# Kernel tuning notes

Measured on AMD Instinct MI355X. Metric: run time of the kernel, lower is better.

## Reference

```python
import jax, jax.numpy as jnp
import numpy as np

K = 8
NEG = -1e16


def setup_inputs() -> dict:
    key = jax.random.key(0)
    inputs = jax.random.normal(key, (1048576, 64), dtype=jnp.float32)
    return {"inputs": inputs}


def reference(inputs) -> jnp.ndarray:
    depth = inputs.shape[1]
    # top-k along last axis (values unused; only indices form the mask)
    _, top_k_indices = jax.lax.top_k(inputs, K)            # [N, K]
    # sum of one-hots -> membership mask [N, depth]
    one_hot = jax.nn.one_hot(top_k_indices, depth, dtype=inputs.dtype)  # [N, K, depth]
    mask = jnp.sum(one_hot, axis=1)                        # [N, depth]
    sparse_inputs = jnp.where(mask > 0.0, inputs, jnp.full_like(inputs, NEG))
    return jax.nn.softmax(sparse_inputs, axis=1)
```

## Files before the change

kernel.cpp:

```cpp
#include <hip/hip_runtime.h>
#include <math.h>


#define D4 16
#define ROWS 32
#define TILE_F4 (ROWS * D4)
#define WAVES 2
#define THREADS (WAVES * 64)

#define LVL(ti) { const float _hi = fmaxf(ti, _a); _a = fminf(ti, _a); ti = _hi; }
#define INSERT(x) { float _a = (x); \
    LVL(t0) LVL(t1) LVL(t2) LVL(t3) LVL(t4) LVL(t5) LVL(t6) \
    t7 = fmaxf(t7, _a); }

#define PROC(x, o) { \
    const int _kgt = ((x) > thr); \
    const int _keq = ((x) == thr) & (quota > 0); \
    quota -= _keq; \
    (o) = (_kgt | _keq) ? __expf((x) - m) * inv : 0.0f; }

__device__ __forceinline__ void gload_lds16(const void* g, void* l) {
    __builtin_amdgcn_global_load_lds(
        (__attribute__((address_space(1))) void*)(g),
        (__attribute__((address_space(3))) void*)(l),
        16, 0, 0);
}

__global__ __launch_bounds__(THREADS)
void topk_softmax_kernel(const float* __restrict__ in,
                         float* __restrict__ out,
                         int ntiles)
{
    __shared__ float4 tile_[WAVES][TILE_F4];

    const int lane = threadIdx.x & 63;
    const int wid  = threadIdx.x >> 6;
    const int w = blockIdx.x * WAVES + wid;
    if (w >= ntiles) return;
    float4* tile = tile_[wid];

    const float4* __restrict__ p = reinterpret_cast<const float4*>(in) + (long long)w * TILE_F4;
    float4* __restrict__ q       = reinterpret_cast<float4*>(out)      + (long long)w * TILE_F4;

    const int g = lane >> 4;
    const int s = lane & 15;

    #pragma unroll
    for (int c = 0; c < 8; ++c) {
        const int r = c * 4 + g;
        const int k = s ^ (r & 15);
        gload_lds16(p + r * 16 + k, tile + c * 64);
    }
    asm volatile("s_waitcnt vmcnt(0)" ::: "memory");

    const int half = lane >> 5;
    const int r    = lane & 31;
    const int kbase = half << 3;
    const int rk = r & 15;
    float4 v[8];
    #pragma unroll
    for (int c = 0; c < 8; ++c) v[c] = tile[r * 16 + ((kbase + c) ^ rk)];

    float t0 = -INFINITY, t1 = -INFINITY, t2 = -INFINITY, t3 = -INFINITY,
          t4 = -INFINITY, t5 = -INFINITY, t6 = -INFINITY, t7 = -INFINITY;
    #pragma unroll
    for (int c = 0; c < 8; ++c) {
        INSERT(v[c].x) INSERT(v[c].y) INSERT(v[c].z) INSERT(v[c].w)
    }

    const float p0 = __shfl_xor(t0, 32), p1 = __shfl_xor(t1, 32),
                p2 = __shfl_xor(t2, 32), p3 = __shfl_xor(t3, 32),
                p4 = __shfl_xor(t4, 32), p5 = __shfl_xor(t5, 32),
                p6 = __shfl_xor(t6, 32), p7 = __shfl_xor(t7, 32);
    const float c0 = fmaxf(t0, p7), c1 = fmaxf(t1, p6), c2 = fmaxf(t2, p5),
                c3 = fmaxf(t3, p4), c4 = fmaxf(t4, p3), c5 = fmaxf(t5, p2),
                c6 = fmaxf(t6, p1), c7 = fmaxf(t7, p0);
    const float m   = fmaxf(t0, p0);
    const float thr = fminf(fminf(fminf(c0, c1), fminf(c2, c3)),
                            fminf(fminf(c4, c5), fminf(c6, c7)));
    const int cnt_gt = (c0 > thr) + (c1 > thr) + (c2 > thr) + (c3 > thr) +
                       (c4 > thr) + (c5 > thr) + (c6 > thr) + (c7 > thr);
    const float sum = __expf(c0 - m) + __expf(c1 - m) + __expf(c2 - m) + __expf(c3 - m) +
                      __expf(c4 - m) + __expf(c5 - m) + __expf(c6 - m) + __expf(c7 - m);
    const float inv = 1.0f / sum;
    const int quota0 = 8 - cnt_gt;

    int ce = 0;
    #pragma unroll
    for (int c = 0; c < 8; ++c)
        ce += (v[c].x == thr) + (v[c].y == thr) + (v[c].z == thr) + (v[c].w == thr);
    const int ce_partner = __shfl_xor(ce, 32);
    int quota = half ? (quota0 - ce_partner) : quota0;

    #pragma unroll
    for (int c = 0; c < 8; ++c) {
        float4 o;
        PROC(v[c].x, o.x) PROC(v[c].y, o.y) PROC(v[c].z, o.z) PROC(v[c].w, o.w)
        tile[r * 16 + ((kbase + c) ^ rk)] = o;
    }
    asm volatile("s_waitcnt lgkmcnt(0)" ::: "memory");

    #pragma unroll
    for (int c = 0; c < 8; ++c) {
        const int rr = c * 4 + g;
        q[c * 64 + lane] = tile[rr * 16 + (s ^ (rr & 15))];
    }
}

__global__ __launch_bounds__(64)
void topk_softmax_tail(const float* __restrict__ in, float* __restrict__ out,
                       long long row0, long long nrows)
{
    const long long row = row0 + threadIdx.x;
    if (row >= nrows) return;
    const float4* __restrict__ p = reinterpret_cast<const float4*>(in) + row * D4;
    float4* __restrict__ q       = reinterpret_cast<float4*>(out)      + row * D4;
    float4 v[D4];
    #pragma unroll
    for (int c = 0; c < D4; ++c) v[c] = p[c];
    float t0 = -INFINITY, t1 = -INFINITY, t2 = -INFINITY, t3 = -INFINITY,
          t4 = -INFINITY, t5 = -INFINITY, t6 = -INFINITY, t7 = -INFINITY;
    #pragma unroll
    for (int c = 0; c < D4; ++c) {
        INSERT(v[c].x) INSERT(v[c].y) INSERT(v[c].z) INSERT(v[c].w)
    }
    const float thr = t7;
    const float m   = t0;
    int quota = 8 - ((t0 > thr) + (t1 > thr) + (t2 > thr) + (t3 > thr) +
                     (t4 > thr) + (t5 > thr) + (t6 > thr));
    const float sum = __expf(t0 - m) + __expf(t1 - m) + __expf(t2 - m) + __expf(t3 - m) +
                      __expf(t4 - m) + __expf(t5 - m) + __expf(t6 - m) + __expf(t7 - m);
    const float inv = 1.0f / sum;
    #pragma unroll
    for (int c = 0; c < D4; ++c) {
        float4 o;
        PROC(v[c].x, o.x) PROC(v[c].y, o.y) PROC(v[c].z, o.z) PROC(v[c].w, o.w)
        q[c] = o;
    }
}

extern "C" void kernel_launch(void* const* d_in, const int* in_sizes, int n_in,
                              void* d_out, int out_size, void* d_ws, size_t ws_size,
                              hipStream_t stream) {
    const float* in = (const float*)d_in[0];
    float* out = (float*)d_out;
    const long long nrows = in_sizes[0] / 64;
    const int ntiles = (int)(nrows / ROWS);
    const long long rem = nrows - (long long)ntiles * ROWS;

    if (ntiles > 0) {
        const int nblocks = (ntiles + WAVES - 1) / WAVES;
        topk_softmax_kernel<<<nblocks, THREADS, 0, stream>>>(in, out, ntiles);
    }
    if (rem > 0) {
        topk_softmax_tail<<<1, 64, 0, stream>>>(in, out, (long long)ntiles * ROWS, nrows);
    }
}
```

Before: 100.6 us.

## Use med3 top-k insertion, log-sum-exp scaling, tie fast path, nontemporal stores

Replaces the min/max insertion network with an fmed3-based sorted insertion, which needs fewer instructions per element. The reciprocal multiply becomes a single subtraction of m+log(sum) inside the exponent. Tie handling now uses a branch-free fast path and runs a slow quota path only when ties straddle the threshold. It also adds occupancy launch bounds and nontemporal output stores. The cost is extra code and small rounding differences from the log-based normalisation.

New measurement: 98.71 us. No clear change (-1.9%).

```diff
diff --git a/kernel.cpp b/kernel.cpp
--- a/kernel.cpp
+++ b/kernel.cpp
@@ -8,11 +8,30 @@
 #define WAVES 2
 #define THREADS (WAVES * 64)
 
+typedef float nfloat4 __attribute__((ext_vector_type(4)));
+
+#define INS(xx) { \
+    const float _x = (xx); \
+    const float n0 = fmaxf(t0, _x); \
+    const float n1 = __builtin_amdgcn_fmed3f(t0, t1, _x); \
+    const float n2 = __builtin_amdgcn_fmed3f(t1, t2, _x); \
+    const float n3 = __builtin_amdgcn_fmed3f(t2, t3, _x); \
+    const float n4 = __builtin_amdgcn_fmed3f(t3, t4, _x); \
+    const float n5 = __builtin_amdgcn_fmed3f(t4, t5, _x); \
+    const float n6 = __builtin_amdgcn_fmed3f(t5, t6, _x); \
+    const float n7 = __builtin_amdgcn_fmed3f(t6, t7, _x); \
+    t0 = n0; t1 = n1; t2 = n2; t3 = n3; t4 = n4; t5 = n5; t6 = n6; t7 = n7; }
+
+#define PROCF(x, o) { (o) = ((x) >= thr) ? __expf((x) - B) : 0.0f; }
+#define PROCS(x, o) { \
+    const int _k = ((x) == thr) & (quota > 0); \
+    quota -= _k; \
+    (o) = (((x) > thr) | _k) ? __expf((x) - B) : 0.0f; }
+
 #define LVL(ti) { const float _hi = fmaxf(ti, _a); _a = fminf(ti, _a); ti = _hi; }
 #define INSERT(x) { float _a = (x); \
     LVL(t0) LVL(t1) LVL(t2) LVL(t3) LVL(t4) LVL(t5) LVL(t6) \
     t7 = fmaxf(t7, _a); }
-
 #define PROC(x, o) { \
     const int _kgt = ((x) > thr); \
     const int _keq = ((x) == thr) & (quota > 0); \
@@ -26,7 +45,7 @@
         16, 0, 0);
 }
 
-__global__ __launch_bounds__(THREADS)
+__global__ __launch_bounds__(THREADS, 5)
 void topk_softmax_kernel(const float* __restrict__ in,
                          float* __restrict__ out,
                          int ntiles)
@@ -48,24 +67,26 @@
     #pragma unroll
     for (int c = 0; c < 8; ++c) {
         const int r = c * 4 + g;
-        const int k = s ^ (r & 15);
-        gload_lds16(p + r * 16 + k, tile + c * 64);
+        gload_lds16(p + r * 16 + (s ^ (r & 15)), tile + c * 64);
     }
     asm volatile("s_waitcnt vmcnt(0)" ::: "memory");
 
-    const int half = lane >> 5;
-    const int r    = lane & 31;
-    const int kbase = half << 3;
+    const int r  = lane & 31;
+    const int h  = lane >> 5;
     const int rk = r & 15;
+    int slot[8];
     float4 v[8];
     #pragma unroll
-    for (int c = 0; c < 8; ++c) v[c] = tile[r * 16 + ((kbase + c) ^ rk)];
+    for (int j = 0; j < 8; ++j) {
+        slot[j] = r * 16 + ((8 * h + j) ^ rk);
+        v[j] = tile[slot[j]];
+    }
 
     float t0 = -INFINITY, t1 = -INFINITY, t2 = -INFINITY, t3 = -INFINITY,
           t4 = -INFINITY, t5 = -INFINITY, t6 = -INFINITY, t7 = -INFINITY;
     #pragma unroll
-    for (int c = 0; c < 8; ++c) {
-        INSERT(v[c].x) INSERT(v[c].y) INSERT(v[c].z) INSERT(v[c].w)
+    for (int j = 0; j < 8; ++j) {
+        INS(v[j].x) INS(v[j].y) INS(v[j].z) INS(v[j].w)
     }
 
     const float p0 = __shfl_xor(t0, 32), p1 = __shfl_xor(t1, 32),
@@ -82,28 +103,51 @@
                        (c4 > thr) + (c5 > thr) + (c6 > thr) + (c7 > thr);
     const float sum = __expf(c0 - m) + __expf(c1 - m) + __expf(c2 - m) + __expf(c3 - m) +
                       __expf(c4 - m) + __expf(c5 - m) + __expf(c6 - m) + __expf(c7 - m);
-    const float inv = 1.0f / sum;
-    const int quota0 = 8 - cnt_gt;
-
-    int ce = 0;
-    #pragma unroll
-    for (int c = 0; c < 8; ++c)
-        ce += (v[c].x == thr) + (v[c].y == thr) + (v[c].z == thr) + (v[c].w == thr);
-    const int ce_partner = __shfl_xor(ce, 32);
-    int quota = half ? (quota0 - ce_partner) : quota0;
-
-    #pragma unroll
-    for (int c = 0; c < 8; ++c) {
+    const float B = m + __logf(sum);
+
+    const int ce8 = (t0 == thr) + (t1 == thr) + (t2 == thr) + (t3 == thr) +
+                    (t4 == thr) + (t5 == thr) + (t6 == thr) + (t7 == thr);
+    const int flags = ce8 | ((t7 == thr) ? 256 : 0);
+    const int pf  = __shfl_xor(flags, 32);
+    const int C   = (flags & 255) + (pf & 255);
+    const int sat = (flags | pf) >> 8;
+    const int qrow = 8 - cnt_gt;
+    const bool slow = (C != qrow) || sat;
+
+    #pragma unroll
+    for (int j = 0; j < 8; ++j) {
         float4 o;
-        PROC(v[c].x, o.x) PROC(v[c].y, o.y) PROC(v[c].z, o.z) PROC(v[c].w, o.w)
-        tile[r * 16 + ((kbase + c) ^ rk)] = o;
+        PROCF(v[j].x, o.x) PROCF(v[j].y, o.y) PROCF(v[j].z, o.z) PROCF(v[j].w, o.w)
+        tile[slot[j]] = o;
+    }
+
+    if (__any(slow)) {
+        if (slow) {
+            int my_eq = 0;
+            #pragma unroll
+            for (int j = 0; j < 8; ++j)
+                my_eq += (v[j].x == thr) + (v[j].y == thr) +
+                         (v[j].z == thr) + (v[j].w == thr);
+            const int peq = __shfl_xor(my_eq, 32);
+            int quota = qrow - (h ? peq : 0);
+            #pragma unroll
+            for (int j = 0; j < 8; ++j) {
+                float4 o;
+                PROCS(v[j].x, o.x) PROCS(v[j].y, o.y)
+                PROCS(v[j].z, o.z) PROCS(v[j].w, o.w)
+                tile[slot[j]] = o;
+            }
+        }
     }
     asm volatile("s_waitcnt lgkmcnt(0)" ::: "memory");
 
     #pragma unroll
     for (int c = 0; c < 8; ++c) {
         const int rr = c * 4 + g;
-        q[c * 64 + lane] = tile[rr * 16 + (s ^ (rr & 15))];
+        const float4 o = tile[rr * 16 + (s ^ (rr & 15))];
+        nfloat4 no; no.x = o.x; no.y = o.y; no.z = o.z; no.w = o.w;
+        __builtin_nontemporal_store(no,
+            reinterpret_cast<nfloat4*>(q + c * 64 + lane));
     }
 }
 
```
